# Performance work log

Hardware: AMD Instinct MI355X
Metric: run time of the kernel (lower is better)

The kernel has to match this reference:

```python
import jax, jax.numpy as jnp
import numpy as np

N_NODES = 50000
N_EDGES = 800000
D_IN = 128
D_OUT = 64

def setup_inputs() -> dict:
    key = jax.random.key(0)
    k1, k2, k3, k4 = jax.random.split(key, 4)
    X = jax.random.normal(k1, (N_NODES, D_IN), dtype=jnp.float32)
    # match torch init: uniform(-stdv, stdv), stdv = 1/sqrt(output_dim)
    stdv = 1.0 / np.sqrt(D_OUT)
    weights = jax.random.uniform(k2, (D_IN, D_OUT), dtype=jnp.float32, minval=-stdv, maxval=stdv)
    # CSR-equivalent edge list: sorted row ids (destination/aggregating node) + column ids (neighbor)
    row_index = jnp.sort(jax.random.randint(k3, (N_EDGES,), 0, N_NODES, dtype=jnp.int32))
    column_index = jax.random.randint(k4, (N_EDGES,), 0, N_NODES, dtype=jnp.int32)
    return {"X": X, "weights": weights, "row_index": row_index, "column_index": column_index}

def reference(X, weights, row_index, column_index):
    # Dense transform: [N, D_in] @ [D_in, D_out] -> [N, D_out]
    X_prime = X @ weights
    # TCGNN CSR SpMM aggregation (unweighted neighbor sum):
    # out[i] = sum_{e: row[e]==i} X_prime[col[e]]
    gathered = X_prime[column_index]  # [E, D_out]
    out = jax.ops.segment_sum(gathered, row_index, num_segments=N_NODES)
    return out
```

## Files before the change

### kernel.cpp

```cpp
#include <hip/hip_runtime.h>
#include <hip/hip_fp16.h>

#define N_NODES 50000
#define D_IN    128
#define D_OUT   64
#define N_EDGES 800000
#define NTILES  (N_NODES / 16)

typedef _Float16 f16x8 __attribute__((ext_vector_type(8)));
typedef float    f32x4 __attribute__((ext_vector_type(4)));

__global__ __launch_bounds__(256) void gemm_xw(const float* __restrict__ X,
                                               const float* __restrict__ W,
                                               _Float16* __restrict__ Xp) {
    __shared__ _Float16 Bf[16 * 64 * 8];

    const int tid = threadIdx.x;
    #pragma unroll
    for (int i = 0; i < 4; ++i) {
        const int p  = tid + 256 * i;
        const int l  = p & 63;
        const int f  = p >> 6;
        const int ct = f >> 2, ks = f & 3;
        const int krow = ks * 32 + (l >> 4) * 8;
        const int col  = ct * 16 + (l & 15);
        f16x8 tmp;
        #pragma unroll
        for (int j = 0; j < 8; ++j)
            tmp[j] = (_Float16)W[(krow + j) * D_OUT + col];
        *reinterpret_cast<f16x8*>(&Bf[p * 8]) = tmp;
    }
    __syncthreads();

    const int wid = (blockIdx.x * 256 + tid) >> 6;
    if (wid >= NTILES) return;
    const int lane = tid & 63;
    const int g    = lane >> 4;
    const int lm   = lane & 15;

    f16x8 bf[16];
    #pragma unroll
    for (int f = 0; f < 16; ++f)
        bf[f] = *reinterpret_cast<const f16x8*>(&Bf[(f * 64 + lane) * 8]);

    const float4* Xrow = reinterpret_cast<const float4*>(X + (size_t)(wid * 16 + lm) * D_IN);
    float4 xa[8];
    #pragma unroll
    for (int ks = 0; ks < 4; ++ks) {
        xa[2 * ks]     = Xrow[ks * 8 + g * 2];
        xa[2 * ks + 1] = Xrow[ks * 8 + g * 2 + 1];
    }

    f32x4 acc[4];
    #pragma unroll
    for (int ct = 0; ct < 4; ++ct) acc[ct] = (f32x4){0.f, 0.f, 0.f, 0.f};

    #pragma unroll
    for (int ks = 0; ks < 4; ++ks) {
        const float xf[8] = {xa[2*ks].x, xa[2*ks].y, xa[2*ks].z, xa[2*ks].w,
                             xa[2*ks+1].x, xa[2*ks+1].y, xa[2*ks+1].z, xa[2*ks+1].w};
        f16x8 ahi, alo;
        #pragma unroll
        for (int j = 0; j < 8; ++j) {
            const _Float16 h = (_Float16)xf[j];
            ahi[j] = h;
            alo[j] = (_Float16)(xf[j] - (float)h);
        }
        #pragma unroll
        for (int ct = 0; ct < 4; ++ct) {
            acc[ct] = __builtin_amdgcn_mfma_f32_16x16x32_f16(ahi, bf[ct * 4 + ks], acc[ct], 0, 0, 0);
            acc[ct] = __builtin_amdgcn_mfma_f32_16x16x32_f16(alo, bf[ct * 4 + ks], acc[ct], 0, 0, 0);
        }
    }

    #pragma unroll
    for (int ct = 0; ct < 4; ++ct)
        #pragma unroll
        for (int r = 0; r < 4; ++r)
            Xp[(size_t)(wid * 16 + g * 4 + r) * D_OUT + ct * 16 + lm] = (_Float16)acc[ct][r];
}

__global__ __launch_bounds__(256) void build_rowptr(const int* __restrict__ row,
                                                    int* __restrict__ rowptr) {
    const int i = blockIdx.x * 256 + threadIdx.x;
    if (i > N_NODES) return;
    int lo = 0, hi = N_EDGES;
    while (lo < hi) {
        int mid = (lo + hi) >> 1;
        if (row[mid] < i) lo = mid + 1; else hi = mid;
    }
    rowptr[i] = lo;
}

__global__ __launch_bounds__(256) void aggregate(const __half* __restrict__ Xp,
                                                 const int* __restrict__ col,
                                                 const int* __restrict__ rowptr,
                                                 float* __restrict__ out) {
    const int wid = (blockIdx.x * 256 + threadIdx.x) >> 6;
    const int j   = threadIdx.x & 63;

    const int lo = rowptr[wid];
    const int hi = rowptr[wid + 1];

    float acc = 0.f;
    int e = lo;
    for (; e + 16 <= hi; e += 16) {
        float v[16];
        #pragma unroll
        for (int q = 0; q < 16; ++q)
            v[q] = __half2float(Xp[(size_t)col[e + q] * D_OUT + j]);
        acc += (((v[0] + v[1]) + (v[2] + v[3])) + ((v[4] + v[5]) + (v[6] + v[7])))
             + (((v[8] + v[9]) + (v[10] + v[11])) + ((v[12] + v[13]) + (v[14] + v[15])));
    }
    for (; e + 4 <= hi; e += 4) {
        float v0 = __half2float(Xp[(size_t)col[e + 0] * D_OUT + j]);
        float v1 = __half2float(Xp[(size_t)col[e + 1] * D_OUT + j]);
        float v2 = __half2float(Xp[(size_t)col[e + 2] * D_OUT + j]);
        float v3 = __half2float(Xp[(size_t)col[e + 3] * D_OUT + j]);
        acc += (v0 + v1) + (v2 + v3);
    }
    for (; e < hi; ++e) {
        acc += __half2float(Xp[(size_t)col[e] * D_OUT + j]);
    }
    out[(size_t)wid * D_OUT + j] = acc;
}

extern "C" void kernel_launch(void* const* d_in, const int* in_sizes, int n_in,
                              void* d_out, int out_size, void* d_ws, size_t ws_size,
                              hipStream_t stream) {
    const float* X   = (const float*)d_in[0];
    const float* W   = (const float*)d_in[1];
    const int*   row = (const int*)d_in[2];
    const int*   col = (const int*)d_in[3];
    float*       out = (float*)d_out;

    _Float16* Xp     = (_Float16*)d_ws;
    int*      rowptr = (int*)((char*)d_ws + (size_t)N_NODES * D_OUT * sizeof(_Float16));

    hipLaunchKernelGGL(gemm_xw, dim3((NTILES + 3) / 4), dim3(256), 0, stream,
                       X, W, Xp);
    hipLaunchKernelGGL(build_rowptr, dim3((N_NODES + 1 + 255) / 256), dim3(256), 0, stream,
                       row, rowptr);
    hipLaunchKernelGGL(aggregate, dim3((N_NODES * 64) / 256), dim3(256), 0, stream,
                       (const __half*)Xp, col, rowptr, out);
}
```

Before: 114.7 us.

## Fuse GEMM with rowptr build, persist GEMM waves, vectorize aggregate with half2 loads

Merges the rowptr binary-search kernel into the GEMM launch as extra blocks, removing one kernel launch and letting both run concurrently. The GEMM becomes a persistent grid-stride loop over tiles that prefetches the next tile's X rows into registers while the current tile's MFMAs run. The aggregate kernel splits each wave into two halves that take alternating edges, with each lane loading a half2 (two features), and combines the halves with a cross-lane shuffle. This halves the gather instructions per edge, but the fixed 256-block persistent grid may underuse the CUs.

```diff
diff --git a/kernel.cpp b/kernel.cpp
--- a/kernel.cpp
+++ b/kernel.cpp
@@ -5,35 +5,51 @@
 #define D_IN    128
 #define D_OUT   64
 #define N_EDGES 800000
-#define NTILES  (N_NODES / 16)
+#define NTILES  3125
+#define GEMM_BLOCKS 256
+#define RP_BLOCKS   196
+#define GEMM_WAVES  (GEMM_BLOCKS * 4)
 
 typedef _Float16 f16x8 __attribute__((ext_vector_type(8)));
 typedef float    f32x4 __attribute__((ext_vector_type(4)));
 
-__global__ __launch_bounds__(256) void gemm_xw(const float* __restrict__ X,
-                                               const float* __restrict__ W,
-                                               _Float16* __restrict__ Xp) {
+__global__ __launch_bounds__(256) void gemm_rowptr(const float* __restrict__ X,
+                                                   const float* __restrict__ W,
+                                                   const int* __restrict__ row,
+                                                   _Float16* __restrict__ Xp,
+                                                   int* __restrict__ rowptr) {
+    const int tid = threadIdx.x;
+
+    if (blockIdx.x >= GEMM_BLOCKS) {
+        const int i = (blockIdx.x - GEMM_BLOCKS) * 256 + tid;
+        if (i <= N_NODES) {
+            int lo = 0, hi = N_EDGES;
+            while (lo < hi) {
+                int mid = (lo + hi) >> 1;
+                if (row[mid] < i) lo = mid + 1; else hi = mid;
+            }
+            rowptr[i] = lo;
+        }
+        return;
+    }
+
     __shared__ _Float16 Bf[16 * 64 * 8];
-
-    const int tid = threadIdx.x;
     #pragma unroll
-    for (int i = 0; i < 4; ++i) {
-        const int p  = tid + 256 * i;
+    for (int i2 = 0; i2 < 4; ++i2) {
+        const int p  = tid + 256 * i2;
         const int l  = p & 63;
         const int f  = p >> 6;
         const int ct = f >> 2, ks = f & 3;
         const int krow = ks * 32 + (l >> 4) * 8;
-        const int col  = ct * 16 + (l & 15);
+        const int c    = ct * 16 + (l & 15);
         f16x8 tmp;
         #pragma unroll
-        for (int j = 0; j < 8; ++j)
-            tmp[j] = (_Float16)W[(krow + j) * D_OUT + col];
+        for (int j = 0; j < 8; ++j) tmp[j] = (_Float16)W[(krow + j) * D_OUT + c];
         *reinterpret_cast<f16x8*>(&Bf[p * 8]) = tmp;
     }
     __syncthreads();
 
-    const int wid = (blockIdx.x * 256 + tid) >> 6;
-    if (wid >= NTILES) return;
+    const int wave = (blockIdx.x * 256 + tid) >> 6;
     const int lane = tid & 63;
     const int g    = lane >> 4;
     const int lm   = lane & 15;
@@ -43,86 +59,111 @@
     for (int f = 0; f < 16; ++f)
         bf[f] = *reinterpret_cast<const f16x8*>(&Bf[(f * 64 + lane) * 8]);
 
-    const float4* Xrow = reinterpret_cast<const float4*>(X + (size_t)(wid * 16 + lm) * D_IN);
+    const float4* X4 = reinterpret_cast<const float4*>(X);
+
+    int t = wave;
     float4 xa[8];
-    #pragma unroll
-    for (int ks = 0; ks < 4; ++ks) {
-        xa[2 * ks]     = Xrow[ks * 8 + g * 2];
-        xa[2 * ks + 1] = Xrow[ks * 8 + g * 2 + 1];
-    }
-
-    f32x4 acc[4];
-    #pragma unroll
-    for (int ct = 0; ct < 4; ++ct) acc[ct] = (f32x4){0.f, 0.f, 0.f, 0.f};
-
-    #pragma unroll
-    for (int ks = 0; ks < 4; ++ks) {
-        const float xf[8] = {xa[2*ks].x, xa[2*ks].y, xa[2*ks].z, xa[2*ks].w,
-                             xa[2*ks+1].x, xa[2*ks+1].y, xa[2*ks+1].z, xa[2*ks+1].w};
-        f16x8 ahi, alo;
+    if (t < NTILES) {
+        const float4* Xr = X4 + (size_t)(t * 16 + lm) * 32;
         #pragma unroll
-        for (int j = 0; j < 8; ++j) {
-            const _Float16 h = (_Float16)xf[j];
-            ahi[j] = h;
-            alo[j] = (_Float16)(xf[j] - (float)h);
-        }
-        #pragma unroll
-        for (int ct = 0; ct < 4; ++ct) {
-            acc[ct] = __builtin_amdgcn_mfma_f32_16x16x32_f16(ahi, bf[ct * 4 + ks], acc[ct], 0, 0, 0);
-            acc[ct] = __builtin_amdgcn_mfma_f32_16x16x32_f16(alo, bf[ct * 4 + ks], acc[ct], 0, 0, 0);
+        for (int ks = 0; ks < 4; ++ks) {
+            xa[2 * ks]     = Xr[ks * 8 + g * 2];
+            xa[2 * ks + 1] = Xr[ks * 8 + g * 2 + 1];
         }
     }
 
-    #pragma unroll
-    for (int ct = 0; ct < 4; ++ct)
+    while (t < NTILES) {
+        const int tn = t + GEMM_WAVES;
+        float4 xb[8];
+        if (tn < NTILES) {
+            const float4* Xr = X4 + (size_t)(tn * 16 + lm) * 32;
+            #pragma unroll
+            for (int ks = 0; ks < 4; ++ks) {
+                xb[2 * ks]     = Xr[ks * 8 + g * 2];
+                xb[2 * ks + 1] = Xr[ks * 8 + g * 2 + 1];
+            }
+        }
+
+        f32x4 acc[4];
         #pragma unroll
-        for (int r = 0; r < 4; ++r)
-            Xp[(size_t)(wid * 16 + g * 4 + r) * D_OUT + ct * 16 + lm] = (_Float16)acc[ct][r];
-}
+        for (int ct = 0; ct < 4; ++ct) acc[ct] = (f32x4){0.f, 0.f, 0.f, 0.f};
 
-__global__ __launch_bounds__(256) void build_rowptr(const int* __restrict__ row,
-                                                    int* __restrict__ rowptr) {
-    const int i = blockIdx.x * 256 + threadIdx.x;
-    if (i > N_NODES) return;
-    int lo = 0, hi = N_EDGES;
-    while (lo < hi) {
-        int mid = (lo + hi) >> 1;
-        if (row[mid] < i) lo = mid + 1; else hi = mid;
+        #pragma unroll
+        for (int ks = 0; ks < 4; ++ks) {
+            const float xf0 = xa[2*ks].x, xf1 = xa[2*ks].y, xf2 = xa[2*ks].z, xf3 = xa[2*ks].w;
+            const float xf4 = xa[2*ks+1].x, xf5 = xa[2*ks+1].y, xf6 = xa[2*ks+1].z, xf7 = xa[2*ks+1].w;
+            f16x8 ahi, alo;
+            ahi[0] = (_Float16)xf0; alo[0] = (_Float16)(xf0 - (float)ahi[0]);
+            ahi[1] = (_Float16)xf1; alo[1] = (_Float16)(xf1 - (float)ahi[1]);
+            ahi[2] = (_Float16)xf2; alo[2] = (_Float16)(xf2 - (float)ahi[2]);
+            ahi[3] = (_Float16)xf3; alo[3] = (_Float16)(xf3 - (float)ahi[3]);
+            ahi[4] = (_Float16)xf4; alo[4] = (_Float16)(xf4 - (float)ahi[4]);
+            ahi[5] = (_Float16)xf5; alo[5] = (_Float16)(xf5 - (float)ahi[5]);
+            ahi[6] = (_Float16)xf6; alo[6] = (_Float16)(xf6 - (float)ahi[6]);
+            ahi[7] = (_Float16)xf7; alo[7] = (_Float16)(xf7 - (float)ahi[7]);
+            #pragma unroll
+            for (int ct = 0; ct < 4; ++ct) {
+                acc[ct] = __builtin_amdgcn_mfma_f32_16x16x32_f16(ahi, bf[ct * 4 + ks], acc[ct], 0, 0, 0);
+                acc[ct] = __builtin_amdgcn_mfma_f32_16x16x32_f16(alo, bf[ct * 4 + ks], acc[ct], 0, 0, 0);
+            }
+        }
+
+        #pragma unroll
+        for (int ct = 0; ct < 4; ++ct)
+            #pragma unroll
+            for (int r = 0; r < 4; ++r)
+                Xp[(size_t)(t * 16 + g * 4 + r) * D_OUT + ct * 16 + lm] = (_Float16)acc[ct][r];
+
+        t = tn;
+        #pragma unroll
+        for (int q = 0; q < 8; ++q) xa[q] = xb[q];
     }
-    rowptr[i] = lo;
 }
 
 __global__ __launch_bounds__(256) void aggregate(const __half* __restrict__ Xp,
                                                  const int* __restrict__ col,
                                                  const int* __restrict__ rowptr,
                                                  float* __restrict__ out) {
-    const int wid = (blockIdx.x * 256 + threadIdx.x) >> 6;
-    const int j   = threadIdx.x & 63;
+    const int wid  = (blockIdx.x * 256 + threadIdx.x) >> 6;
+    const int lane = threadIdx.x & 63;
+    const int h    = lane >> 5;
+    const int c2   = lane & 31;
 
     const int lo = rowptr[wid];
     const int hi = rowptr[wid + 1];
 
-    float acc = 0.f;
-    int e = lo;
+    const uint* Xp32 = reinterpret_cast<const uint*>(Xp);
+    float ax = 0.f, ay = 0.f;
+
+    int e = lo + h;
     for (; e + 16 <= hi; e += 16) {
-        float v[16];
+        int c[8];
         #pragma unroll
-        for (int q = 0; q < 16; ++q)
-            v[q] = __half2float(Xp[(size_t)col[e + q] * D_OUT + j]);
-        acc += (((v[0] + v[1]) + (v[2] + v[3])) + ((v[4] + v[5]) + (v[6] + v[7])))
-             + (((v[8] + v[9]) + (v[10] + v[11])) + ((v[12] + v[13]) + (v[14] + v[15])));
+        for (int q = 0; q < 8; ++q) c[q] = col[e + 2 * q];
+        uint u[8];
+        #pragma unroll
+        for (int q = 0; q < 8; ++q) u[q] = Xp32[(size_t)c[q] * 32 + c2];
+        #pragma unroll
+        for (int q = 0; q < 8; ++q) {
+            const __half2 hv = *reinterpret_cast<const __half2*>(&u[q]);
+            const float2  f  = __half22float2(hv);
+            ax += f.x; ay += f.y;
+        }
     }
-    for (; e + 4 <= hi; e += 4) {
-        float v0 = __half2float(Xp[(size_t)col[e + 0] * D_OUT + j]);
-        float v1 = __half2float(Xp[(size_t)col[e + 1] * D_OUT + j]);
-        float v2 = __half2float(Xp[(size_t)col[e + 2] * D_OUT + j]);
-        float v3 = __half2float(Xp[(size_t)col[e + 3] * D_OUT + j]);
-        acc += (v0 + v1) + (v2 + v3);
+    for (; e < hi; e += 2) {
+        const uint u = Xp32[(size_t)col[e] * 32 + c2];
+        const __half2 hv = *reinterpret_cast<const __half2*>(&u);
+        const float2  f  = __half22float2(hv);
+        ax += f.x; ay += f.y;
     }
-    for (; e < hi; ++e) {
-        acc += __half2float(Xp[(size_t)col[e] * D_OUT + j]);
+
+    ax += __shfl_xor(ax, 32, 64);
+    ay += __shfl_xor(ay, 32, 64);
+
+    if (h == 0) {
+        float2 v; v.x = ax; v.y = ay;
+        *reinterpret_cast<float2*>(&out[(size_t)wid * D_OUT + c2 * 2]) = v;
     }
-    out[(size_t)wid * D_OUT + j] = acc;
 }
 
 extern "C" void kernel_launch(void* const* d_in, const int* in_sizes, int n_in,
@@ -137,10 +178,8 @@
     _Float16* Xp     = (_Float16*)d_ws;
     int*      rowptr = (int*)((char*)d_ws + (size_t)N_NODES * D_OUT * sizeof(_Float16));
 
-    hipLaunchKernelGGL(gemm_xw, dim3((NTILES + 3) / 4), dim3(256), 0, stream,
-                       X, W, Xp);
-    hipLaunchKernelGGL(build_rowptr, dim3((N_NODES + 1 + 255) / 256), dim3(256), 0, stream,
-                       row, rowptr);
+    hipLaunchKernelGGL(gemm_rowptr, dim3(GEMM_BLOCKS + RP_BLOCKS), dim3(256), 0, stream,
+                       X, W, row, Xp, rowptr);
     hipLaunchKernelGGL(aggregate, dim3((N_NODES * 64) / 256), dim3(256), 0, stream,
                        (const __half*)Xp, col, rowptr, out);
 }
```

New measurement: 115.1 us. About the same (+0.4%).
